# Kernel optimization log

Measured on AMD Instinct MI355X. Metric: run time of the kernel, lower is better.

Reference implementation:

```python
import jax, jax.numpy as jnp
import numpy as np

B, T, C = 32, 256, 512
MAX_LEN = 25


def setup_inputs() -> dict:
    key = jax.random.key(0)
    ks = jax.random.split(key, 6)
    scale = 1.0 / np.sqrt(C)
    return {
        "word_features": jax.random.normal(ks[0], (B, T, C), dtype=jnp.float32),
        "word_fc_w": jax.random.normal(ks[1], (C, C), dtype=jnp.float32) * scale,
        "word_fc_b": jax.random.normal(ks[2], (C,), dtype=jnp.float32) * scale,
        "pos_emb": jax.random.normal(ks[3], (MAX_LEN, C), dtype=jnp.float32),
        "atten_w": jax.random.normal(ks[4], (C,), dtype=jnp.float32) * scale,
        "atten_b": jax.random.normal(ks[5], (1,), dtype=jnp.float32) * scale,
    }


def reference(word_features, word_fc_w, word_fc_b, pos_emb, atten_w, atten_b):
    # word_fc: (b,t,c) -> (b,t,c)
    wf = jnp.einsum("btc,dc->btd", word_features, word_fc_w) + word_fc_b
    # additive (Bahdanau) attention scores over t for each of max_len query positions
    # add_features: (b, L, t, c) = wf[:,None,:,:] + pos_emb[None,:,None,:]
    add_features = jnp.tanh(wf[:, None, :, :] + pos_emb[None, :, None, :])
    # atten_fc: (b, L, t, 1) -> squeeze -> (b, L, t)
    scores = jnp.einsum("bltc,c->blt", add_features, atten_w) + atten_b[0]
    attn = jax.nn.softmax(scores, axis=2)  # softmax over t
    # bmm: (b,L,t) @ (b,t,c) -> (b,L,c)
    pvam_features = jnp.einsum("blt,btc->blc", attn, wf)
    return pvam_features
```

## Files before the change

### kernel.cpp

```cpp
#include <hip/hip_runtime.h>

#define Bn 32
#define Tn 256
#define Cn 512
#define Ln 25

typedef _Float16 h8 __attribute__((ext_vector_type(8)));
typedef _Float16 h4 __attribute__((ext_vector_type(4)));
typedef __attribute__((ext_vector_type(4))) float f32x4;

#define SCALE2LOG2E 2.885390081777927f

#if __has_builtin(__builtin_amdgcn_exp2f)
#define EXP2(x) __builtin_amdgcn_exp2f(x)
#else
#define EXP2(x) __expf(0.69314718056f * (x))
#endif

#define DPP_ADD(v, ctrl) \
    ((v) + __int_as_float(__builtin_amdgcn_update_dpp(0, __float_as_int(v), ctrl, 0xf, 0xf, true)))

#define NW_OCT (Cn * Cn / 8)
#define NP_OCT (Ln * Cn / 8)
__global__ __launch_bounds__(256) void k_convert(
        const float* __restrict__ W, const float* __restrict__ pos,
        _Float16* __restrict__ W2, float* __restrict__ EP) {
    int idx = blockIdx.x * 256 + threadIdx.x;
    if (idx < NW_OCT) {
        int off = idx * 8;
        float4 v0 = *(const float4*)&W[off];
        float4 v1 = *(const float4*)&W[off + 4];
        h8 o;
        o[0] = (_Float16)v0.x; o[1] = (_Float16)v0.y;
        o[2] = (_Float16)v0.z; o[3] = (_Float16)v0.w;
        o[4] = (_Float16)v1.x; o[5] = (_Float16)v1.y;
        o[6] = (_Float16)v1.z; o[7] = (_Float16)v1.w;
        *(h8*)&W2[off] = o;
    } else if (idx < NW_OCT + NP_OCT) {
        int off = (idx - NW_OCT) * 8;
        float4 v0 = *(const float4*)&pos[off];
        float4 v1 = *(const float4*)&pos[off + 4];
        float4 t0, t1;
        t0.x = EXP2(SCALE2LOG2E * v0.x); t0.y = EXP2(SCALE2LOG2E * v0.y);
        t0.z = EXP2(SCALE2LOG2E * v0.z); t0.w = EXP2(SCALE2LOG2E * v0.w);
        t1.x = EXP2(SCALE2LOG2E * v1.x); t1.y = EXP2(SCALE2LOG2E * v1.y);
        t1.z = EXP2(SCALE2LOG2E * v1.z); t1.w = EXP2(SCALE2LOG2E * v1.w);
        *(float4*)&EP[off] = t0;
        *(float4*)&EP[off + 4] = t1;
    }
}

#define BM 128
#define BN 64
#define BKg 64
__global__ __launch_bounds__(256) void k_gemm(
        const float* __restrict__ A, const _Float16* __restrict__ W2,
        const float* __restrict__ bias, _Float16* __restrict__ wf) {
    __shared__ _Float16 As[BM * BKg];
    __shared__ _Float16 Ws[BN * BKg];
    const int tid  = threadIdx.x;
    const int lane = tid & 63;
    const int wv   = tid >> 6;
    const int m0 = blockIdx.y * BM;
    const int n0 = blockIdx.x * BN;
    const int wm = (wv >> 1) * 64;
    const int wn = (wv & 1) * 32;
    const int r = lane & 15, q = lane >> 4;

    const float* gA[4];
    const _Float16* gW[2];
    #pragma unroll
    for (int rr = 0; rr < 4; ++rr) {
        int p = rr * 256 + tid;
        int row = p >> 3, pk = p & 7;
        int lk = pk ^ (row & 7);
        gA[rr] = A + (size_t)(m0 + row) * Cn + lk * 8;
    }
    #pragma unroll
    for (int rr = 0; rr < 2; ++rr) {
        int p = rr * 256 + tid;
        int row = p >> 3, pk = p & 7;
        int lk = pk ^ (row & 7);
        gW[rr] = W2 + (size_t)(n0 + row) * Cn + lk * 8;
    }

    f32x4 acc[4][2];
    #pragma unroll
    for (int mi = 0; mi < 4; ++mi)
        #pragma unroll
        for (int ni = 0; ni < 2; ++ni) acc[mi][ni] = (f32x4){0.f, 0.f, 0.f, 0.f};

    for (int kt = 0; kt < Cn / BKg; ++kt) {
        float4 va[4], vb[4];
        #pragma unroll
        for (int rr = 0; rr < 4; ++rr) {
            va[rr] = *(const float4*)gA[rr];
            vb[rr] = *(const float4*)(gA[rr] + 4);
            gA[rr] += BKg;
        }
        __syncthreads();
        #pragma unroll
        for (int rr = 0; rr < 2; ++rr) {
            __builtin_amdgcn_global_load_lds(
                (const __attribute__((address_space(1))) unsigned int*)gW[rr],
                (__attribute__((address_space(3))) unsigned int*)(Ws + (rr * 256 + wv * 64) * 8),
                16, 0, 0);
            gW[rr] += BKg;
        }
        #pragma unroll
        for (int rr = 0; rr < 4; ++rr) {
            h8 o;
            o[0] = (_Float16)va[rr].x; o[1] = (_Float16)va[rr].y;
            o[2] = (_Float16)va[rr].z; o[3] = (_Float16)va[rr].w;
            o[4] = (_Float16)vb[rr].x; o[5] = (_Float16)vb[rr].y;
            o[6] = (_Float16)vb[rr].z; o[7] = (_Float16)vb[rr].w;
            *(h8*)&As[(rr * 256 + tid) * 8] = o;
        }
        __syncthreads();

        h8 af[4][2], bfr[2][2];
        #pragma unroll
        for (int mi = 0; mi < 4; ++mi)
            #pragma unroll
            for (int kk = 0; kk < 2; ++kk) {
                int row = wm + mi * 16 + r;
                int phys = (kk * 4 + q) ^ (r & 7);
                af[mi][kk] = *(const h8*)&As[row * BKg + phys * 8];
            }
        #pragma unroll
        for (int ni = 0; ni < 2; ++ni)
            #pragma unroll
            for (int kk = 0; kk < 2; ++kk) {
                int row = wn + ni * 16 + r;
                int phys = (kk * 4 + q) ^ (r & 7);
                bfr[ni][kk] = *(const h8*)&Ws[row * BKg + phys * 8];
            }
        #pragma unroll
        for (int kk = 0; kk < 2; ++kk)
            #pragma unroll
            for (int mi = 0; mi < 4; ++mi)
                #pragma unroll
                for (int ni = 0; ni < 2; ++ni)
                    acc[mi][ni] = __builtin_amdgcn_mfma_f32_16x16x32_f16(
                        af[mi][kk], bfr[ni][kk], acc[mi][ni], 0, 0, 0);
    }

    #pragma unroll
    for (int ni = 0; ni < 2; ++ni) {
        const float bv = bias[n0 + wn + ni * 16 + r];
        #pragma unroll
        for (int mi = 0; mi < 4; ++mi)
            #pragma unroll
            for (int reg = 0; reg < 4; ++reg) {
                int row = m0 + wm + mi * 16 + q * 4 + reg;
                int col = n0 + wn + ni * 16 + r;
                wf[(size_t)row * Cn + col] = (_Float16)(acc[mi][ni][reg] + bv);
            }
    }
}

__global__ __launch_bounds__(512) void k_scores(
        const _Float16* __restrict__ wf, const float* __restrict__ EP,
        const float* __restrict__ aw, float* __restrict__ scores) {
    __shared__ float part[4 * Ln * 8];
    const int tid  = threadIdx.x;
    const int lane = tid & 63;
    const int wv   = tid >> 6;
    const int tl   = wv >> 1;
    const int ch   = wv & 1;
    const int t    = blockIdx.x * 4 + tl;
    const int b    = blockIdx.y;
    const int co   = ch * 256 + lane * 4;

    const h4 wh = *(const h4*)&wf[(size_t)(b * Tn + t) * Cn + co];
    float4 ew;
    ew.x = EXP2(SCALE2LOG2E * (float)wh[0]);
    ew.y = EXP2(SCALE2LOG2E * (float)wh[1]);
    ew.z = EXP2(SCALE2LOG2E * (float)wh[2]);
    ew.w = EXP2(SCALE2LOG2E * (float)wh[3]);
    float4 a = *(const float4*)&aw[co];
    a.x *= -2.f; a.y *= -2.f; a.z *= -2.f; a.w *= -2.f;

    const float* pp = EP + co;
    float* prt = &part[tl * Ln * 8 + ch * 4 + (lane >> 4)];
    const bool writer = ((lane & 15) == 0);

    #pragma unroll
    for (int lo = 0; lo < 5; ++lo) {
        float4 pv[5];
        #pragma unroll
        for (int j = 0; j < 5; ++j)
            pv[j] = *(const float4*)(pp + (lo * 5 + j) * Cn);
        #pragma unroll
        for (int j = 0; j < 5; ++j) {
            const float4 p = pv[j];
            float d0 = fmaf(ew.x, p.x, 1.f);
            float s  = a.x * __builtin_amdgcn_rcpf(d0);
            float d1 = fmaf(ew.y, p.y, 1.f);
            s = fmaf(a.y, __builtin_amdgcn_rcpf(d1), s);
            float d2 = fmaf(ew.z, p.z, 1.f);
            s = fmaf(a.z, __builtin_amdgcn_rcpf(d2), s);
            float d3 = fmaf(ew.w, p.w, 1.f);
            s = fmaf(a.w, __builtin_amdgcn_rcpf(d3), s);
            s = DPP_ADD(s, 0xB1);
            s = DPP_ADD(s, 0x4E);
            s = DPP_ADD(s, 0x141);
            s = DPP_ADD(s, 0x140);
            if (writer) prt[(lo * 5 + j) * 8] = s;
        }
    }
    __syncthreads();
    if (tid < 4 * Ln) {
        int tl2 = tid / Ln, l2 = tid - tl2 * Ln;
        const float* q = &part[(tl2 * Ln + l2) * 8];
        float v = ((q[0] + q[1]) + (q[2] + q[3])) + ((q[4] + q[5]) + (q[6] + q[7]));
        scores[(b * Ln + l2) * Tn + blockIdx.x * 4 + tl2] = v;
    }
}

__global__ __launch_bounds__(512) void k_pvam(
        const _Float16* __restrict__ wf, const float* __restrict__ scores,
        float* __restrict__ out) {
    __shared__ float buf[8 * Ln * 64];
    __shared__ float pT[Tn][28];
    const int tid = threadIdx.x;
    const int cx  = blockIdx.x;
    const int b   = blockIdx.y;

    const float* sc = scores + b * Ln * Tn;
    for (int i = tid * 4; i < Ln * Tn; i += 2048)
        *(float4*)&buf[i] = *(const float4*)&sc[i];
    __syncthreads();

    const int lane = tid & 63;
    const int wv   = tid >> 6;

    for (int l = wv; l < Ln; l += 8) {
        float v0 = buf[l * Tn + lane];
        float v1 = buf[l * Tn + 64 + lane];
        float v2 = buf[l * Tn + 128 + lane];
        float v3 = buf[l * Tn + 192 + lane];
        float m = fmaxf(fmaxf(v0, v1), fmaxf(v2, v3));
        #pragma unroll
        for (int o = 32; o > 0; o >>= 1) m = fmaxf(m, __shfl_xor(m, o));
        float e0 = __expf(v0 - m), e1 = __expf(v1 - m);
        float e2 = __expf(v2 - m), e3 = __expf(v3 - m);
        float s = e0 + e1 + e2 + e3;
        #pragma unroll
        for (int o = 32; o > 0; o >>= 1) s += __shfl_xor(s, o);
        float rs = __builtin_amdgcn_rcpf(s);
        pT[lane][l]       = e0 * rs;
        pT[64 + lane][l]  = e1 * rs;
        pT[128 + lane][l] = e2 * rs;
        pT[192 + lane][l] = e3 * rs;
    }
    __syncthreads();

    const int c = cx * 64 + lane;
    float acc[Ln];
    #pragma unroll
    for (int l = 0; l < Ln; ++l) acc[l] = 0.f;

    const _Float16* wfp = wf + (size_t)(b * Tn + wv * 32) * Cn + c;
    for (int tt = 0; tt < 32; ++tt) {
        float w = (float)wfp[(size_t)tt * Cn];
        const float* pp = &pT[wv * 32 + tt][0];
        float p[Ln];
        *(float4*)&p[0]  = *(const float4*)&pp[0];
        *(float4*)&p[4]  = *(const float4*)&pp[4];
        *(float4*)&p[8]  = *(const float4*)&pp[8];
        *(float4*)&p[12] = *(const float4*)&pp[12];
        *(float4*)&p[16] = *(const float4*)&pp[16];
        *(float4*)&p[20] = *(const float4*)&pp[20];
        p[24] = pp[24];
        #pragma unroll
        for (int l = 0; l < Ln; ++l) acc[l] = fmaf(p[l], w, acc[l]);
    }

    __syncthreads();
    #pragma unroll
    for (int l = 0; l < Ln; ++l)
        buf[(wv * Ln + l) * 64 + lane] = acc[l];
    __syncthreads();
    for (int idx = tid; idx < Ln * 64; idx += 512) {
        int l = idx >> 6, cc = idx & 63;
        float v = 0.f;
        #pragma unroll
        for (int w = 0; w < 8; ++w) v += buf[(w * Ln + l) * 64 + cc];
        out[(b * Ln + l) * Cn + cx * 64 + cc] = v;
    }
}

extern "C" void kernel_launch(void* const* d_in, const int* in_sizes, int n_in,
                              void* d_out, int out_size, void* d_ws, size_t ws_size,
                              hipStream_t stream) {
    const float* A    = (const float*)d_in[0];
    const float* W    = (const float*)d_in[1];
    const float* bias = (const float*)d_in[2];
    const float* pos  = (const float*)d_in[3];
    const float* aw   = (const float*)d_in[4];

    char* ws = (char*)d_ws;
    _Float16*  wf     = (_Float16*)ws;
    float*     scores = (float*)(ws + 8388608ull);
    _Float16*  W2     = (_Float16*)(ws + 9207808ull);
    float*     EP     = (float*)(ws + 9732096ull);
    float* out = (float*)d_out;

    const int nconv = (NW_OCT + NP_OCT + 255) / 256;
    k_convert<<<nconv, 256, 0, stream>>>(W, pos, W2, EP);
    k_gemm<<<dim3(Cn / BN, (Bn * Tn) / BM), 256, 0, stream>>>(A, W2, bias, wf);
    k_scores<<<dim3(Tn / 4, Bn), 512, 0, stream>>>(wf, EP, aw, scores);
    k_pvam<<<dim3(Cn / 64, Bn), 512, 0, stream>>>(wf, scores, out);
}
```

Before: 123.0 us.

## Fuse weight conversion and pos-exp into GEMM, register-prefetch next K tile

Removes the separate conversion kernel: the GEMM now reads fp32 weights directly and converts them to fp16 in registers, and a few blocks of the GEMM compute the exponentiated positional table. The main loop is restructured to prefetch the next K-tile of A and W into registers while the current one is stored to LDS, overlapping global loads with compute. This saves one launch and the round trip of the fp16 weight copy. In exchange, each GEMM block redundantly converts W tiles, reads twice the weight bytes, and uses more registers.

```diff
diff --git a/kernel.cpp b/kernel.cpp
--- a/kernel.cpp
+++ b/kernel.cpp
@@ -20,45 +20,35 @@
 #define DPP_ADD(v, ctrl) \
     ((v) + __int_as_float(__builtin_amdgcn_update_dpp(0, __float_as_int(v), ctrl, 0xf, 0xf, true)))
 
-#define NW_OCT (Cn * Cn / 8)
 #define NP_OCT (Ln * Cn / 8)
-__global__ __launch_bounds__(256) void k_convert(
-        const float* __restrict__ W, const float* __restrict__ pos,
-        _Float16* __restrict__ W2, float* __restrict__ EP) {
-    int idx = blockIdx.x * 256 + threadIdx.x;
-    if (idx < NW_OCT) {
-        int off = idx * 8;
-        float4 v0 = *(const float4*)&W[off];
-        float4 v1 = *(const float4*)&W[off + 4];
-        h8 o;
-        o[0] = (_Float16)v0.x; o[1] = (_Float16)v0.y;
-        o[2] = (_Float16)v0.z; o[3] = (_Float16)v0.w;
-        o[4] = (_Float16)v1.x; o[5] = (_Float16)v1.y;
-        o[6] = (_Float16)v1.z; o[7] = (_Float16)v1.w;
-        *(h8*)&W2[off] = o;
-    } else if (idx < NW_OCT + NP_OCT) {
-        int off = (idx - NW_OCT) * 8;
-        float4 v0 = *(const float4*)&pos[off];
-        float4 v1 = *(const float4*)&pos[off + 4];
-        float4 t0, t1;
-        t0.x = EXP2(SCALE2LOG2E * v0.x); t0.y = EXP2(SCALE2LOG2E * v0.y);
-        t0.z = EXP2(SCALE2LOG2E * v0.z); t0.w = EXP2(SCALE2LOG2E * v0.w);
-        t1.x = EXP2(SCALE2LOG2E * v1.x); t1.y = EXP2(SCALE2LOG2E * v1.y);
-        t1.z = EXP2(SCALE2LOG2E * v1.z); t1.w = EXP2(SCALE2LOG2E * v1.w);
-        *(float4*)&EP[off] = t0;
-        *(float4*)&EP[off + 4] = t1;
-    }
-}
 
 #define BM 128
 #define BN 64
 #define BKg 64
 __global__ __launch_bounds__(256) void k_gemm(
-        const float* __restrict__ A, const _Float16* __restrict__ W2,
-        const float* __restrict__ bias, _Float16* __restrict__ wf) {
+        const float* __restrict__ A, const float* __restrict__ W,
+        const float* __restrict__ bias, const float* __restrict__ pos,
+        _Float16* __restrict__ wf, float* __restrict__ EP) {
     __shared__ _Float16 As[BM * BKg];
     __shared__ _Float16 Ws[BN * BKg];
     const int tid  = threadIdx.x;
+
+    if (blockIdx.y == 0 && blockIdx.x < 7) {
+        int idx = blockIdx.x * 256 + tid;
+        if (idx < NP_OCT) {
+            int off = idx * 8;
+            float4 v0 = *(const float4*)&pos[off];
+            float4 v1 = *(const float4*)&pos[off + 4];
+            float4 t0, t1;
+            t0.x = EXP2(SCALE2LOG2E * v0.x); t0.y = EXP2(SCALE2LOG2E * v0.y);
+            t0.z = EXP2(SCALE2LOG2E * v0.z); t0.w = EXP2(SCALE2LOG2E * v0.w);
+            t1.x = EXP2(SCALE2LOG2E * v1.x); t1.y = EXP2(SCALE2LOG2E * v1.y);
+            t1.z = EXP2(SCALE2LOG2E * v1.z); t1.w = EXP2(SCALE2LOG2E * v1.w);
+            *(float4*)&EP[off] = t0;
+            *(float4*)&EP[off + 4] = t1;
+        }
+    }
+
     const int lane = tid & 63;
     const int wv   = tid >> 6;
     const int m0 = blockIdx.y * BM;
@@ -68,7 +58,7 @@
     const int r = lane & 15, q = lane >> 4;
 
     const float* gA[4];
-    const _Float16* gW[2];
+    const float* gW[2];
     #pragma unroll
     for (int rr = 0; rr < 4; ++rr) {
         int p = rr * 256 + tid;
@@ -81,7 +71,7 @@
         int p = rr * 256 + tid;
         int row = p >> 3, pk = p & 7;
         int lk = pk ^ (row & 7);
-        gW[rr] = W2 + (size_t)(n0 + row) * Cn + lk * 8;
+        gW[rr] = W + (size_t)(n0 + row) * Cn + lk * 8;
     }
 
     f32x4 acc[4][2];
@@ -90,32 +80,60 @@
         #pragma unroll
         for (int ni = 0; ni < 2; ++ni) acc[mi][ni] = (f32x4){0.f, 0.f, 0.f, 0.f};
 
+    float4 va[4], vb[4], vc[2], vd[2];
+    #pragma unroll
+    for (int rr = 0; rr < 4; ++rr) {
+        va[rr] = *(const float4*)gA[rr];
+        vb[rr] = *(const float4*)(gA[rr] + 4);
+        gA[rr] += BKg;
+    }
+    #pragma unroll
+    for (int rr = 0; rr < 2; ++rr) {
+        vc[rr] = *(const float4*)gW[rr];
+        vd[rr] = *(const float4*)(gW[rr] + 4);
+        gW[rr] += BKg;
+    }
+
     for (int kt = 0; kt < Cn / BKg; ++kt) {
-        float4 va[4], vb[4];
+        h8 oa[4], ow[2];
         #pragma unroll
         for (int rr = 0; rr < 4; ++rr) {
-            va[rr] = *(const float4*)gA[rr];
-            vb[rr] = *(const float4*)(gA[rr] + 4);
-            gA[rr] += BKg;
-        }
+            oa[rr][0] = (_Float16)va[rr].x; oa[rr][1] = (_Float16)va[rr].y;
+            oa[rr][2] = (_Float16)va[rr].z; oa[rr][3] = (_Float16)va[rr].w;
+            oa[rr][4] = (_Float16)vb[rr].x; oa[rr][5] = (_Float16)vb[rr].y;
+            oa[rr][6] = (_Float16)vb[rr].z; oa[rr][7] = (_Float16)vb[rr].w;
+        }
+        #pragma unroll
+        for (int rr = 0; rr < 2; ++rr) {
+            ow[rr][0] = (_Float16)vc[rr].x; ow[rr][1] = (_Float16)vc[rr].y;
+            ow[rr][2] = (_Float16)vc[rr].z; ow[rr][3] = (_Float16)vc[rr].w;
+            ow[rr][4] = (_Float16)vd[rr].x; ow[rr][5] = (_Float16)vd[rr].y;
+            ow[rr][6] = (_Float16)vd[rr].z; ow[rr][7] = (_Float16)vd[rr].w;
+        }
+
         __syncthreads();
-        #pragma unroll
-        for (int rr = 0; rr < 2; ++rr) {
-            __builtin_amdgcn_global_load_lds(
-                (const __attribute__((address_space(1))) unsigned int*)gW[rr],
-                (__attribute__((address_space(3))) unsigned int*)(Ws + (rr * 256 + wv * 64) * 8),
-                16, 0, 0);
-            gW[rr] += BKg;
-        }
-        #pragma unroll
-        for (int rr = 0; rr < 4; ++rr) {
-            h8 o;
-            o[0] = (_Float16)va[rr].x; o[1] = (_Float16)va[rr].y;
-            o[2] = (_Float16)va[rr].z; o[3] = (_Float16)va[rr].w;
-            o[4] = (_Float16)vb[rr].x; o[5] = (_Float16)vb[rr].y;
-            o[6] = (_Float16)vb[rr].z; o[7] = (_Float16)vb[rr].w;
-            *(h8*)&As[(rr * 256 + tid) * 8] = o;
-        }
+
+        if (kt + 1 < Cn / BKg) {
+            #pragma unroll
+            for (int rr = 0; rr < 4; ++rr) {
+                va[rr] = *(const float4*)gA[rr];
+                vb[rr] = *(const float4*)(gA[rr] + 4);
+                gA[rr] += BKg;
+            }
+            #pragma unroll
+            for (int rr = 0; rr < 2; ++rr) {
+                vc[rr] = *(const float4*)gW[rr];
+                vd[rr] = *(const float4*)(gW[rr] + 4);
+                gW[rr] += BKg;
+            }
+        }
+
+        #pragma unroll
+        for (int rr = 0; rr < 4; ++rr)
+            *(h8*)&As[(rr * 256 + tid) * 8] = oa[rr];
+        #pragma unroll
+        for (int rr = 0; rr < 2; ++rr)
+            *(h8*)&Ws[(rr * 256 + tid) * 8] = ow[rr];
         __syncthreads();
 
         h8 af[4][2], bfr[2][2];
@@ -303,13 +321,10 @@
     char* ws = (char*)d_ws;
     _Float16*  wf     = (_Float16*)ws;
     float*     scores = (float*)(ws + 8388608ull);
-    _Float16*  W2     = (_Float16*)(ws + 9207808ull);
-    float*     EP     = (float*)(ws + 9732096ull);
+    float*     EP     = (float*)(ws + 9207808ull);
     float* out = (float*)d_out;
 
-    const int nconv = (NW_OCT + NP_OCT + 255) / 256;
-    k_convert<<<nconv, 256, 0, stream>>>(W, pos, W2, EP);
-    k_gemm<<<dim3(Cn / BN, (Bn * Tn) / BM), 256, 0, stream>>>(A, W2, bias, wf);
+    k_gemm<<<dim3(Cn / BN, (Bn * Tn) / BM), 256, 0, stream>>>(A, W, bias, pos, wf, EP);
     k_scores<<<dim3(Tn / 4, Bn), 512, 0, stream>>>(wf, EP, aw, scores);
     k_pvam<<<dim3(Cn / 64, Bn), 512, 0, stream>>>(wf, scores, out);
 }
```

After: 120.4 us. 2.1% less time.
